# Optimization experiments

Hardware: AMD Instinct MI355X
Metric: run time of the kernel (lower is better)

Reference implementation:

```python
import jax, jax.numpy as jnp
import numpy as np

N = 20000      # nodes
E = 400000     # edges
D = 256        # input_dim == hidden_dim
L = 4          # num_layers
EIN = 32       # edgenet_input_dim // 2
EH = 128       # edge parser hidden
NC = 2         # num_classes
JK = L * D     # 1024
BN_EPS = 1e-5


def setup_inputs() -> dict:
    key = jax.random.key(0)
    ks = jax.random.split(key, 16)
    s = 0.05
    inp = {
        "features": jax.random.normal(ks[0], (N, D), jnp.float32),
        "edge_index": jax.random.randint(ks[1], (2, E), 0, N, dtype=jnp.int64),
        "edgenet_input": jax.random.normal(ks[2], (E, 2 * EIN), jnp.float32),
        # ChebConv weights: [layer, k, in, out] (all layers 256->256, K=3, no bias)
        "cheb_w": jax.random.normal(ks[3], (L, 3, D, D), jnp.float32) * s,
        # EdgeEncoder (PAE-style) parser: Linear(32,128)+ReLU+BN+Linear(128,128)
        "en_w1": jax.random.normal(ks[4], (EIN, EH), jnp.float32) * s,
        "en_b1": jnp.zeros((EH,), jnp.float32),
        "en_g1": jnp.ones((EH,), jnp.float32),
        "en_be1": jnp.zeros((EH,), jnp.float32),
        "en_w2": jax.random.normal(ks[5], (EH, EH), jnp.float32) * s,
        "en_b2": jnp.zeros((EH,), jnp.float32),
        # cls head: Linear(1024,256)+ReLU+BN(256)+Linear(256,2)
        "cls_w1": jax.random.normal(ks[6], (JK, 256), jnp.float32) * s,
        "cls_b1": jnp.zeros((256,), jnp.float32),
        "cls_g": jnp.ones((256,), jnp.float32),
        "cls_b": jnp.zeros((256,), jnp.float32),
        "cls_w2": jax.random.normal(ks[7], (256, NC), jnp.float32) * s,
        "cls_b2": jnp.zeros((NC,), jnp.float32),
    }
    return inp


def _bn_eval(x, g, b):
    # eval-mode BatchNorm1d with fresh running stats (mean=0, var=1)
    return x * (g / jnp.sqrt(1.0 + BN_EPS)) + b


def reference(features, edge_index, edgenet_input, cheb_w,
              en_w1, en_b1, en_g1, en_be1, en_w2, en_b2,
              cls_w1, cls_b1, cls_g, cls_b, cls_w2, cls_b2):
    row, col = edge_index[0], edge_index[1]

    # ---- EdgeEncoder (PAE): shared parser on both halves + cosine sim ----
    def parser(x):
        h = jnp.maximum(x @ en_w1 + en_b1, 0.0)
        h = _bn_eval(h, en_g1, en_be1)
        return h @ en_w2 + en_b2

    half = edgenet_input.shape[1] // 2
    h1 = parser(edgenet_input[:, :half])
    h2 = parser(edgenet_input[:, half:])
    n1 = jnp.maximum(jnp.linalg.norm(h1, axis=1), 1e-8)
    n2 = jnp.maximum(jnp.linalg.norm(h2, axis=1), 1e-8)
    cos = jnp.sum(h1 * h2, axis=1) / (n1 * n2)
    edge_weight = (cos + 1.0) * 0.5  # [E]

    # ---- ChebConv sym normalization (lambda_max=2): L_hat = -D^-1/2 A D^-1/2 ----
    deg = jax.ops.segment_sum(edge_weight, row, num_segments=N)
    dis = jnp.where(deg > 0, jax.lax.rsqrt(jnp.maximum(deg, 1e-30)), 0.0)
    norm = -dis[row] * edge_weight * dis[col]  # [E]

    def prop(x):  # out[col] += norm * x[row]
        return jax.ops.segment_sum(x[row] * norm[:, None], col, num_segments=N)

    # ---- stacked ChebConv (K=3, no bias) + ReLU + JK concat ----
    x = features
    jk = None
    for i in range(L):
        W = cheb_w[i]
        Tx0 = x
        Tx1 = prop(Tx0)
        Tx2 = 2.0 * prop(Tx1) - Tx0
        h = jnp.maximum(Tx0 @ W[0] + Tx1 @ W[1] + Tx2 @ W[2], 0.0)
        jk = h if i == 0 else jnp.concatenate([jk, h], axis=1)
        x = h

    # ---- cls head ----
    z = jnp.maximum(jk @ cls_w1 + cls_b1, 0.0)
    z = _bn_eval(z, cls_g, cls_b)
    logit = z @ cls_w2 + cls_b2
    return (logit, edge_weight)
```

## Files before the change

### kernel.cpp

```cpp
#include <hip/hip_runtime.h>
#include <hip/hip_bf16.h>

#define NN 20000
#define EE 400000
#define RSBN 0.9999950000374997f

typedef __attribute__((ext_vector_type(8))) short short8;
typedef __attribute__((ext_vector_type(8))) unsigned short ushort8;
typedef __attribute__((ext_vector_type(4))) short bf4;
typedef __attribute__((ext_vector_type(4))) float floatx4;

__device__ __forceinline__ short f2bf(float f) {
  union { float f; unsigned u; } v; v.f = f;
  unsigned r = v.u + 0x7fffu + ((v.u >> 16) & 1u);
  return (short)(r >> 16);
}
__device__ __forceinline__ unsigned f2bf2(float x, float y) {
  union { __hip_bfloat162 h; unsigned u; } v;
  v.h = __float22bfloat162_rn(make_float2(x, y));
  return v.u;
}
__device__ __forceinline__ float bf2f(unsigned short u) {
  union { unsigned u; float f; } v; v.u = ((unsigned)u) << 16;
  return v.f;
}
__device__ __forceinline__ void gl_lds16(const void* g, void* l) {
  __builtin_amdgcn_global_load_lds(
      (const __attribute__((address_space(1))) unsigned*)g,
      (__attribute__((address_space(3))) unsigned*)l, 16, 0, 0);
}

__device__ __forceinline__ floatx4 mfma16(bf4 a, bf4 b, floatx4 c) {
#if __has_builtin(__builtin_amdgcn_mfma_f32_16x16x16bf16_1k)
  return __builtin_amdgcn_mfma_f32_16x16x16bf16_1k(a, b, c, 0, 0, 0);
#else
  floatx4 d;
  asm volatile("v_mfma_f32_16x16x16_bf16 %0, %1, %2, %3"
               : "=&v"(d) : "v"(a), "v"(b), "v"(c));
  return d;
#endif
}

__device__ __forceinline__ float dpp_xor1(float x) {
  union { float f; int i; } a, b;
  a.f = x;
  b.i = __builtin_amdgcn_update_dpp(0, a.i, 0xB1, 0xF, 0xF, false);
  return b.f;
}

__global__ __launch_bounds__(256) void ewconv_kernel(
    const float* __restrict__ w1, const float* __restrict__ w2,
    const float* __restrict__ g1, const float* __restrict__ be1,
    const float* __restrict__ b1, const float* __restrict__ b2,
    unsigned short* __restrict__ ewf)
{
  int tid = threadIdx.x;
#pragma unroll
  for (int i = 0; i < 16; i++) {
    int idx = i * 256 + tid;
    int k = idx >> 7, n = idx & 127;
    int pos = ((n >> 4) * 64 + (k >> 3) * 16 + (n & 15)) * 8 + (k & 7);
    ewf[pos] = f2bf(w1[idx]);
  }
#pragma unroll
  for (int i = 0; i < 64; i++) {
    int idx = i * 256 + tid;
    int k = idx >> 7, n = idx & 127;
    int u = k >> 4, q = (k >> 2) & 3, j = k & 3;
    int t = n >> 4, l = n & 15;
    int pos = (((u * 8 + t) * 4 + q) * 16 + l) * 4 + j;
    ewf[4096 + pos] = f2bf(w2[idx] * g1[k] * RSBN);
  }
  float* fb = (float*)(ewf + 20480);
  if (tid < 128) {
    fb[tid] = b1[tid];
    float acc = b2[tid];
    for (int k = 0; k < 128; k++) acc += be1[k] * w2[k * 128 + tid] * g1[k] * RSBN;
    fb[128 + tid] = acc;
  }
}

__global__ __launch_bounds__(512, 4) void edge_kernel(
    const float* __restrict__ xin, const int* __restrict__ eidx,
    const unsigned short* __restrict__ ewf,
    float* __restrict__ ew_out,
    float* __restrict__ deg, int* __restrict__ cnt)
{
  __shared__ short wbuf[20992];

  int tid = threadIdx.x;
  int lane = tid & 63;
  int wv = tid >> 6;
  int l15 = lane & 15;
  int quad = lane >> 4;

#pragma unroll
  for (int i = 0; i < 5; i++)
    gl_lds16(ewf + (i * 512 + tid) * 8, &wbuf[(i * 512 + tid) * 8]);
  if (tid < 64)
    gl_lds16(ewf + (2560 + tid) * 8, &wbuf[(2560 + tid) * 8]);

  const short* w1f = wbuf;
  const short* w2f = wbuf + 4096;

  int rowA = blockIdx.x * 256 + wv * 16;
  int rowB = rowA + 128;

  short8 afA, afB;
  {
    const float* xpA = xin + (size_t)(rowA + l15) * 32 + quad * 8;
    const float* xpB = xin + (size_t)(rowB + l15) * 32 + quad * 8;
    float4 a0 = *(const float4*)xpA;
    float4 a1 = *(const float4*)(xpA + 4);
    float4 b0 = *(const float4*)xpB;
    float4 b1v = *(const float4*)(xpB + 4);
    union { short8 s; unsigned u[4]; } a, b;
    a.u[0] = f2bf2(a0.x, a0.y); a.u[1] = f2bf2(a0.z, a0.w);
    a.u[2] = f2bf2(a1.x, a1.y); a.u[3] = f2bf2(a1.z, a1.w);
    b.u[0] = f2bf2(b0.x, b0.y); b.u[1] = f2bf2(b0.z, b0.w);
    b.u[2] = f2bf2(b1v.x, b1v.y); b.u[3] = f2bf2(b1v.z, b1v.w);
    afA = a.s; afB = b.s;
  }

  __syncthreads();

  const float* fb = (const float*)(wbuf + 20480);

  floatx4 acc1A[8], acc1B[8];
#pragma unroll
  for (int t = 0; t < 8; t++) {
    floatx4 z = *(const floatx4*)&fb[t * 16 + quad * 4];
    short8 w1v = *(const short8*)&w1f[(t * 64 + lane) * 8];
    acc1A[t] = __builtin_amdgcn_mfma_f32_16x16x32_bf16(w1v, afA, z, 0, 0, 0);
    acc1B[t] = __builtin_amdgcn_mfma_f32_16x16x32_bf16(w1v, afB, z, 0, 0, 0);
  }

  bf4 pbA[8], pbB[8];
#pragma unroll
  for (int u = 0; u < 8; u++) {
    union { bf4 s; unsigned w[2]; } oa, ob;
    oa.w[0] = f2bf2(fmaxf(acc1A[u][0], 0.f), fmaxf(acc1A[u][1], 0.f));
    oa.w[1] = f2bf2(fmaxf(acc1A[u][2], 0.f), fmaxf(acc1A[u][3], 0.f));
    ob.w[0] = f2bf2(fmaxf(acc1B[u][0], 0.f), fmaxf(acc1B[u][1], 0.f));
    ob.w[1] = f2bf2(fmaxf(acc1B[u][2], 0.f), fmaxf(acc1B[u][3], 0.f));
    pbA[u] = oa.s; pbB[u] = ob.s;
  }

  floatx4 acc2A[8], acc2B[8];
#pragma unroll
  for (int t = 0; t < 8; t++) {
    floatx4 z2 = *(const floatx4*)&fb[128 + t * 16 + quad * 4];
    acc2A[t] = z2; acc2B[t] = z2;
  }
#pragma unroll
  for (int u = 0; u < 8; u++)
#pragma unroll
    for (int t = 0; t < 8; t++) {
      bf4 a4 = *(const bf4*)&w2f[((u * 8 + t) * 64 + lane) * 4];
      acc2A[t] = mfma16(a4, pbA[u], acc2A[t]);
      acc2B[t] = mfma16(a4, pbB[u], acc2B[t]);
    }

#pragma unroll
  for (int tile = 0; tile < 2; tile++) {
    floatx4* acc2 = tile ? acc2B : acc2A;
    int rowbase = tile ? rowB : rowA;
    float qq = 0.f, pp = 0.f;
#pragma unroll
    for (int t = 0; t < 8; t++)
#pragma unroll
      for (int r = 0; r < 4; r++) {
        float h = acc2[t][r];
        float hp = dpp_xor1(h);
        qq += h * h;
        pp += h * hp;
      }
    qq += __shfl_xor(qq, 16, 64);
    pp += __shfl_xor(pp, 16, 64);
    qq += __shfl_xor(qq, 32, 64);
    pp += __shfl_xor(pp, 32, 64);
    float rr = dpp_xor1(qq);

    if (quad == 0 && !(l15 & 1)) {
      int e = (rowbase + l15) >> 1;
      float n1 = fmaxf(sqrtf(qq), 1e-8f);
      float n2 = fmaxf(sqrtf(rr), 1e-8f);
      float w = (pp / (n1 * n2) + 1.f) * 0.5f;
      ew_out[e] = w;
      atomicAdd(deg + eidx[e], w);
      atomicAdd(cnt + eidx[EE + e], 1);
    }
  }
}

__global__ __launch_bounds__(256) void fconv_kernel(const float* __restrict__ src,
                                                    unsigned short* __restrict__ dst) {
  size_t i = ((size_t)blockIdx.x * 256 + threadIdx.x) * 8;
  float4 a = *(const float4*)(src + i);
  float4 b = *(const float4*)(src + i + 4);
  union { ushort8 s; unsigned u[4]; } o;
  o.u[0] = f2bf2(a.x, a.y); o.u[1] = f2bf2(a.z, a.w);
  o.u[2] = f2bf2(b.x, b.y); o.u[3] = f2bf2(b.z, b.w);
  *(ushort8*)(dst + i) = o.s;
}

__global__ __launch_bounds__(256) void wconv_kernel(
    const float* __restrict__ cheb_w, const float* __restrict__ cls_w1,
    unsigned short* __restrict__ wtc, unsigned short* __restrict__ clsT)
{
  __shared__ unsigned short tile[64][80];
  int z = blockIdx.z;
  const float* src; unsigned short* dst; int ldk;
  if (z < 12) {
    int l = z / 3, c = z % 3;
    src = cheb_w + (size_t)z * 65536;
    dst = wtc + (size_t)l * 196608 + c * 256;
    ldk = 768;
  } else {
    int c = z - 12;
    src = cls_w1 + (size_t)c * 65536;
    dst = clsT + c * 256;
    ldk = 1024;
  }
  int t = threadIdx.x;
  int k0 = blockIdx.x * 64, n0 = blockIdx.y * 64;
#pragma unroll
  for (int pass = 0; pass < 4; pass++) {
    int kk = pass * 16 + (t >> 4);
    int nl = (t & 15) * 4;
    float4 v = *(const float4*)(src + (size_t)(k0 + kk) * 256 + n0 + nl);
    tile[nl + 0][kk] = f2bf(v.x);
    tile[nl + 1][kk] = f2bf(v.y);
    tile[nl + 2][kk] = f2bf(v.z);
    tile[nl + 3][kk] = f2bf(v.w);
  }
  __syncthreads();
  int nl = t >> 2, kc = (t & 3) * 16;
  ushort8 v0 = *(const ushort8*)&tile[nl][kc];
  ushort8 v1 = *(const ushort8*)&tile[nl][kc + 8];
  unsigned short* dp = dst + (size_t)(n0 + nl) * ldk + k0 + kc;
  *(ushort8*)dp = v0;
  *(ushort8*)(dp + 8) = v1;
}

__global__ __launch_bounds__(1024) void scan_kernel(const int* __restrict__ cnt, int* __restrict__ ptr) {
  __shared__ int sums[1024];
  int tid = threadIdx.x;
  const int n = NN;
  const int chunk = (n + 1023) / 1024;
  int base = tid * chunk;
  int s = 0;
  for (int i = 0; i < chunk; i++) {
    int idx = base + i;
    if (idx < n) s += (cnt[idx] + 3) & ~3;
  }
  sums[tid] = s;
  __syncthreads();
  for (int off = 1; off < 1024; off <<= 1) {
    int v = (tid >= off) ? sums[tid - off] : 0;
    __syncthreads();
    sums[tid] += v;
    __syncthreads();
  }
  int run = (tid == 0) ? 0 : sums[tid - 1];
  for (int i = 0; i < chunk; i++) {
    int idx = base + i;
    if (idx < n) { ptr[idx] = run; run += (cnt[idx] + 3) & ~3; }
  }
  if (tid == 1023) ptr[n] = run;
}

__global__ __launch_bounds__(256) void hist_kernel(const int* __restrict__ cnt,
                                                   int* __restrict__ hist) {
  __shared__ int lh[64];
  int tid = threadIdx.x;
  if (tid < 64) lh[tid] = 0;
  __syncthreads();
  int i = blockIdx.x * 256 + tid;
  if (i < NN) {
    int b = (cnt[i] + 3) >> 2; if (b > 63) b = 63;
    atomicAdd(&lh[b], 1);
  }
  __syncthreads();
  if (tid < 64 && lh[tid]) atomicAdd(&hist[tid], lh[tid]);
}

__global__ void binscan_kernel(const int* __restrict__ hist,
                               int* __restrict__ binbase, int* __restrict__ binfill) {
  int tid = threadIdx.x;
  int v = hist[tid];
  int x = v;
#pragma unroll
  for (int off = 1; off < 64; off <<= 1) {
    int y = __shfl_up(x, off, 64);
    if (tid >= off) x += y;
  }
  binbase[tid] = x - v;
  binfill[tid] = 0;
}

__global__ __launch_bounds__(256) void perm_kernel(const int* __restrict__ cnt,
                                                   const int* __restrict__ binbase,
                                                   int* __restrict__ binfill,
                                                   int* __restrict__ perm) {
  __shared__ int lh[64], lbase[64];
  int tid = threadIdx.x;
  if (tid < 64) lh[tid] = 0;
  __syncthreads();
  int i = blockIdx.x * 256 + tid;
  int b = 0, local = 0;
  bool valid = (i < NN);
  if (valid) {
    b = (cnt[i] + 3) >> 2; if (b > 63) b = 63;
    local = atomicAdd(&lh[b], 1);
  }
  __syncthreads();
  if (tid < 64 && lh[tid]) lbase[tid] = atomicAdd(&binfill[tid], lh[tid]);
  __syncthreads();
  if (valid) perm[binbase[b] + lbase[b] + local] = i;
}

__global__ void fill_kernel(const int* __restrict__ eidx, const float* __restrict__ ew,
                            const float* __restrict__ deg, const int* __restrict__ ptr,
                            int* __restrict__ fill, int* __restrict__ cidx, float* __restrict__ cval) {
  int e = blockIdx.x * 256 + threadIdx.x;
  if (e < EE) {
    int r = eidx[e], c = eidx[EE + e];
    float dr = deg[r], dc = deg[c];
    float ir = dr > 0.f ? 1.f / sqrtf(fmaxf(dr, 1e-30f)) : 0.f;
    float ic = dc > 0.f ? 1.f / sqrtf(fmaxf(dc, 1e-30f)) : 0.f;
    float nv = -ir * ew[e] * ic;
    int pos = ptr[c] + atomicAdd(&fill[c], 1);
    cidx[pos] = r;
    cval[pos] = nv;
  }
}

__global__ __launch_bounds__(256) void prop_kernel(
    const unsigned short* __restrict__ x, int ldx,
    const int* __restrict__ cidx, const float* __restrict__ cval,
    const int* __restrict__ ptr, const int* __restrict__ perm,
    unsigned short* __restrict__ y, int ldy,
    float alpha, const unsigned short* __restrict__ sub, int ldsub)
{
  int sliceid = blockIdx.x & 7;
  int colslice = sliceid >> 1;
  int chunk = (blockIdx.x >> 3) * 2 + (sliceid & 1);
  int ci = chunk * 32 + (threadIdx.x >> 3);
  if (ci >= NN) return;
  int c = perm[ci];
  int d = colslice * 64 + (threadIdx.x & 7) * 8;
  int p0 = ptr[c], p1 = ptr[c + 1];
  float a[8] = {0.f, 0.f, 0.f, 0.f, 0.f, 0.f, 0.f, 0.f};

#define PLOAD(P, R, W, V0, V1, V2, V3)                                  \
  do {                                                                  \
    R = *(const int4*)(cidx + (P));                                     \
    W = *(const float4*)(cval + (P));                                   \
    V0 = *(const ushort8*)(x + (size_t)R.x * ldx + d);                  \
    V1 = *(const ushort8*)(x + (size_t)R.y * ldx + d);                  \
    V2 = *(const ushort8*)(x + (size_t)R.z * ldx + d);                  \
    V3 = *(const ushort8*)(x + (size_t)R.w * ldx + d);                  \
  } while (0)

#define PACC(W, V0, V1, V2, V3)                                         \
  do {                                                                  \
    _Pragma("unroll")                                                   \
    for (int j = 0; j < 8; j++)                                         \
      a[j] += W.x * bf2f(V0[j]) + W.y * bf2f(V1[j]) +                   \
              W.z * bf2f(V2[j]) + W.w * bf2f(V3[j]);                    \
  } while (0)

  if (p0 < p1) {
    int n4 = (p1 - p0) >> 2;
    int4 rA, rB; float4 wA, wB;
    ushort8 vA0, vA1, vA2, vA3, vB0, vB1, vB2, vB3;
    PLOAD(p0, rA, wA, vA0, vA1, vA2, vA3);
    if (n4 == 1) {
      PACC(wA, vA0, vA1, vA2, vA3);
    } else {
      PLOAD(p0 + 4, rB, wB, vB0, vB1, vB2, vB3);
      int p = p0 + 8;
      if (n4 & 1) {
        PACC(wA, vA0, vA1, vA2, vA3);
        PLOAD(p, rA, wA, vA0, vA1, vA2, vA3);
        p += 4;
      }
      for (; p < p1; p += 8) {
        PACC(wA, vA0, vA1, vA2, vA3);
        PLOAD(p, rA, wA, vA0, vA1, vA2, vA3);
        PACC(wB, vB0, vB1, vB2, vB3);
        PLOAD(p + 4, rB, wB, vB0, vB1, vB2, vB3);
      }
      PACC(wA, vA0, vA1, vA2, vA3);
      PACC(wB, vB0, vB1, vB2, vB3);
    }
  }
#undef PLOAD
#undef PACC

  union { ushort8 s; unsigned u[4]; } o;
  if (sub) {
    ushort8 sv = *(const ushort8*)(sub + (size_t)c * ldsub + d);
#pragma unroll
    for (int j = 0; j < 8; j += 2)
      o.u[j >> 1] = f2bf2(alpha * a[j] - bf2f(sv[j]), alpha * a[j + 1] - bf2f(sv[j + 1]));
  } else {
#pragma unroll
    for (int j = 0; j < 8; j += 2)
      o.u[j >> 1] = f2bf2(a[j], a[j + 1]);
  }
  *(ushort8*)(y + (size_t)c * ldy + d) = o.s;
}

__global__ __launch_bounds__(256, 4) void mgemm_kernel(
    const unsigned short* A0, const unsigned short* A1,
    const unsigned short* A2, const unsigned short* A3,
    int l0, int l1, int l2, int l3, int nchunks,
    const unsigned short* __restrict__ BT, int ldbt,
    unsigned short* __restrict__ Cb, float* __restrict__ Cf, int ldc, int M,
    const float* __restrict__ bias, const float* __restrict__ bng,
    const float* __restrict__ bnb)
{
  __shared__ short As[4 * 64 * 8];
  __shared__ short Bs[4 * 128 * 8];
  int tid = threadIdx.x;
  int lane = tid & 63;
  int wv = tid >> 6;
  int l15 = lane & 15, quad = lane >> 4;
  int wr = wv >> 1, wc = wv & 1;
  int m0 = blockIdx.x * 64, n0 = blockIdx.y * 128;

  const unsigned short* Ap[4] = {A0, A1, A2, A3};
  int Al[4] = {l0, l1, l2, l3};

  int arow = tid & 63, ac = tid >> 6;
  int brow = tid & 127, bc = tid >> 7;

  floatx4 acc[2][4];
#pragma unroll
  for (int mi = 0; mi < 2; mi++)
#pragma unroll
    for (int nj = 0; nj < 4; nj++) acc[mi][nj] = (floatx4){0.f, 0.f, 0.f, 0.f};

  for (int c = 0; c < nchunks; c++) {
    const unsigned short* Abase = Ap[c] + (size_t)(m0 + arow) * Al[c] + ac * 8;
    const unsigned short* Bbase = BT + (size_t)(n0 + brow) * ldbt + c * 256 + bc * 8;
#pragma unroll 1
    for (int kb = 0; kb < 256; kb += 32) {
      __syncthreads();
      gl_lds16(Abase + kb, &As[tid * 8]);
      gl_lds16(Bbase + kb, &Bs[tid * 8]);
      gl_lds16(Bbase + 16 + kb, &Bs[(tid + 256) * 8]);
      __syncthreads();
      short8 af[2], bfv[4];
#pragma unroll
      for (int mi = 0; mi < 2; mi++)
        af[mi] = *(const short8*)&As[(quad * 64 + wr * 32 + mi * 16 + l15) * 8];
#pragma unroll
      for (int nj = 0; nj < 4; nj++)
        bfv[nj] = *(const short8*)&Bs[(quad * 128 + wc * 64 + nj * 16 + l15) * 8];
#pragma unroll
      for (int nj = 0; nj < 4; nj++)
#pragma unroll
        for (int mi = 0; mi < 2; mi++)
          acc[mi][nj] = __builtin_amdgcn_mfma_f32_16x16x32_bf16(af[mi], bfv[nj], acc[mi][nj], 0, 0, 0);
    }
  }

  if (Cb) {
#pragma unroll
    for (int mi = 0; mi < 2; mi++)
#pragma unroll
      for (int r = 0; r < 4; r++) {
        int row = m0 + wr * 32 + mi * 16 + quad * 4 + r;
        if (row < M) {
#pragma unroll
          for (int nj = 0; nj < 4; nj++) {
            int col = n0 + wc * 64 + nj * 16 + l15;
            Cb[(size_t)row * ldc + col] = (unsigned short)f2bf(fmaxf(acc[mi][nj][r], 0.f));
          }
        }
      }
  } else {
    float bs[4], g[4], bb[4];
#pragma unroll
    for (int nj = 0; nj < 4; nj++) {
      int col = n0 + wc * 64 + nj * 16 + l15;
      bs[nj] = bias[col]; g[nj] = bng[col] * RSBN; bb[nj] = bnb[col];
    }
#pragma unroll
    for (int mi = 0; mi < 2; mi++)
#pragma unroll
      for (int r = 0; r < 4; r++) {
        int row = m0 + wr * 32 + mi * 16 + quad * 4 + r;
        if (row < M) {
#pragma unroll
          for (int nj = 0; nj < 4; nj++) {
            int col = n0 + wc * 64 + nj * 16 + l15;
            float v = fmaxf(acc[mi][nj][r] + bs[nj], 0.f) * g[nj] + bb[nj];
            Cf[(size_t)row * ldc + col] = v;
          }
        }
      }
  }
}

__global__ __launch_bounds__(256) void logit_kernel(
    const float* __restrict__ z, const float* __restrict__ w2,
    const float* __restrict__ b2, float* __restrict__ out)
{
  int node = blockIdx.x * 4 + (threadIdx.x >> 6);
  if (node >= NN) return;
  int lane = threadIdx.x & 63;
  int k = lane * 4;
  float4 zv = *(const float4*)(z + (size_t)node * 256 + k);
  float4 wa = *(const float4*)(w2 + k * 2);
  float4 wb = *(const float4*)(w2 + k * 2 + 4);
  float a0 = zv.x * wa.x + zv.y * wa.z + zv.z * wb.x + zv.w * wb.z;
  float a1 = zv.x * wa.y + zv.y * wa.w + zv.z * wb.y + zv.w * wb.w;
#pragma unroll
  for (int m = 32; m >= 1; m >>= 1) {
    a0 += __shfl_xor(a0, m, 64);
    a1 += __shfl_xor(a1, m, 64);
  }
  if (lane == 0) {
    out[(size_t)node * 2]     = a0 + b2[0];
    out[(size_t)node * 2 + 1] = a1 + b2[1];
  }
}

extern "C" void kernel_launch(void* const* d_in, const int* in_sizes, int n_in,
                              void* d_out, int out_size, void* d_ws, size_t ws_size,
                              hipStream_t stream) {
  const float* features = (const float*)d_in[0];
  const int*   eidx     = (const int*)d_in[1];
  const float* xin      = (const float*)d_in[2];
  const float* cheb_w   = (const float*)d_in[3];
  const float* en_w1    = (const float*)d_in[4];
  const float* en_b1    = (const float*)d_in[5];
  const float* en_g1    = (const float*)d_in[6];
  const float* en_be1   = (const float*)d_in[7];
  const float* en_w2    = (const float*)d_in[8];
  const float* en_b2    = (const float*)d_in[9];
  const float* cls_w1   = (const float*)d_in[10];
  const float* cls_b1   = (const float*)d_in[11];
  const float* cls_g    = (const float*)d_in[12];
  const float* cls_b    = (const float*)d_in[13];
  const float* cls_w2   = (const float*)d_in[14];
  const float* cls_b2   = (const float*)d_in[15];
  float* out = (float*)d_out;

  char* ws = (char*)d_ws;
  size_t off = 0;
  auto alloc = [&](size_t bytes) -> void* {
    void* p = ws + off;
    off += (bytes + 255) & ~(size_t)255;
    return p;
  };
  const int CSRN = EE + 4 * NN;
  float* deg  = (float*)alloc((size_t)NN * 4);
  int*   cnt  = (int*)  alloc((size_t)NN * 4);
  int*   fil  = (int*)  alloc((size_t)NN * 4);
  int*   hist = (int*)  alloc(64 * 4);
  float* cval = (float*)alloc((size_t)CSRN * 4);
  int*   cidx = (int*)  alloc((size_t)CSRN * 4);
  size_t zero_len = off;
  int*   ptr  = (int*)  alloc((size_t)(NN + 1) * 4);
  int*   perm = (int*)  alloc((size_t)NN * 4);
  int*   binbase = (int*)alloc(64 * 4);
  int*   binfill = (int*)alloc(64 * 4);
  unsigned short* featb = (unsigned short*)alloc((size_t)NN * 256 * 2);
  unsigned short* Tx1   = (unsigned short*)alloc((size_t)NN * 256 * 2);
  unsigned short* Tx2   = (unsigned short*)alloc((size_t)NN * 256 * 2);
  unsigned short* jk    = (unsigned short*)alloc((size_t)NN * 1024 * 2);
  float* zbuf = (float*)alloc((size_t)NN * 256 * 4);
  unsigned short* wtc   = (unsigned short*)alloc((size_t)4 * 196608 * 2);
  unsigned short* clsT  = (unsigned short*)alloc((size_t)256 * 1024 * 2);
  unsigned short* ewf   = (unsigned short*)alloc((size_t)20992 * 2);
  alloc(262144);

  float* ew = out + (size_t)NN * 2;

  hipMemsetAsync(deg, 0, zero_len, stream);

  ewconv_kernel<<<1, 256, 0, stream>>>(en_w1, en_w2, en_g1, en_be1, en_b1, en_b2, ewf);
  edge_kernel<<<3125, 512, 0, stream>>>(xin, eidx, ewf, ew, deg, cnt);
  fconv_kernel<<<2500, 256, 0, stream>>>(features, featb);
  wconv_kernel<<<dim3(4, 4, 16), 256, 0, stream>>>(cheb_w, cls_w1, wtc, clsT);
  scan_kernel<<<1, 1024, 0, stream>>>(cnt, ptr);
  hist_kernel<<<(NN + 255) / 256, 256, 0, stream>>>(cnt, hist);
  binscan_kernel<<<1, 64, 0, stream>>>(hist, binbase, binfill);
  perm_kernel<<<(NN + 255) / 256, 256, 0, stream>>>(cnt, binbase, binfill, perm);
  fill_kernel<<<(EE + 255) / 256, 256, 0, stream>>>(eidx, ew, deg, ptr, fil, cidx, cval);

  dim3 ggrid(313, 2);
  for (int i = 0; i < 4; i++) {
    const unsigned short* x = (i == 0) ? featb : (jk + (size_t)(i - 1) * 256);
    int ldx = (i == 0) ? 256 : 1024;
    prop_kernel<<<2504, 256, 0, stream>>>(x, ldx, cidx, cval, ptr, perm, Tx1, 256, 1.f, nullptr, 0);
    prop_kernel<<<2504, 256, 0, stream>>>(Tx1, 256, cidx, cval, ptr, perm, Tx2, 256, 2.f, x, ldx);
    mgemm_kernel<<<ggrid, 256, 0, stream>>>(x, Tx1, Tx2, nullptr, ldx, 256, 256, 0, 3,
                                            wtc + (size_t)i * 196608, 768,
                                            jk + (size_t)i * 256, nullptr, 1024, NN,
                                            nullptr, nullptr, nullptr);
  }

  mgemm_kernel<<<ggrid, 256, 0, stream>>>(jk, jk + 256, jk + 512, jk + 768,
                                          1024, 1024, 1024, 1024, 4, clsT, 1024,
                                          nullptr, zbuf, 256, NN,
                                          cls_b1, cls_g, cls_b);
  logit_kernel<<<NN / 4, 256, 0, stream>>>(zbuf, cls_w2, cls_b2, out);
}
```

Baseline: 648.2 us.

## Simplify prop gather loop, raise its occupancy, and XCD-swizzle GEMM blocks

```diff
diff --git a/kernel.cpp b/kernel.cpp
--- a/kernel.cpp
+++ b/kernel.cpp
@@ -46,6 +46,12 @@
   a.f = x;
   b.i = __builtin_amdgcn_update_dpp(0, a.i, 0xB1, 0xF, 0xF, false);
   return b.f;
+}
+
+__device__ __forceinline__ int xcd_swizzle(int bid, int nwg) {
+  int q = nwg >> 3, r = nwg & 7;
+  int x = bid & 7, o = bid >> 3;
+  return (x < r ? x * (q + 1) : r * (q + 1) + (x - r) * q) + o;
 }
 
 __global__ __launch_bounds__(256) void ewconv_kernel(
@@ -336,7 +342,7 @@
   }
 }
 
-__global__ __launch_bounds__(256) void prop_kernel(
+__global__ __launch_bounds__(256, 8) void prop_kernel(
     const unsigned short* __restrict__ x, int ldx,
     const int* __restrict__ cidx, const float* __restrict__ cval,
     const int* __restrict__ ptr, const int* __restrict__ perm,
@@ -353,51 +359,18 @@
   int p0 = ptr[c], p1 = ptr[c + 1];
   float a[8] = {0.f, 0.f, 0.f, 0.f, 0.f, 0.f, 0.f, 0.f};
 
-#define PLOAD(P, R, W, V0, V1, V2, V3)                                  \
-  do {                                                                  \
-    R = *(const int4*)(cidx + (P));                                     \
-    W = *(const float4*)(cval + (P));                                   \
-    V0 = *(const ushort8*)(x + (size_t)R.x * ldx + d);                  \
-    V1 = *(const ushort8*)(x + (size_t)R.y * ldx + d);                  \
-    V2 = *(const ushort8*)(x + (size_t)R.z * ldx + d);                  \
-    V3 = *(const ushort8*)(x + (size_t)R.w * ldx + d);                  \
-  } while (0)
-
-#define PACC(W, V0, V1, V2, V3)                                         \
-  do {                                                                  \
-    _Pragma("unroll")                                                   \
-    for (int j = 0; j < 8; j++)                                         \
-      a[j] += W.x * bf2f(V0[j]) + W.y * bf2f(V1[j]) +                   \
-              W.z * bf2f(V2[j]) + W.w * bf2f(V3[j]);                    \
-  } while (0)
-
-  if (p0 < p1) {
-    int n4 = (p1 - p0) >> 2;
-    int4 rA, rB; float4 wA, wB;
-    ushort8 vA0, vA1, vA2, vA3, vB0, vB1, vB2, vB3;
-    PLOAD(p0, rA, wA, vA0, vA1, vA2, vA3);
-    if (n4 == 1) {
-      PACC(wA, vA0, vA1, vA2, vA3);
-    } else {
-      PLOAD(p0 + 4, rB, wB, vB0, vB1, vB2, vB3);
-      int p = p0 + 8;
-      if (n4 & 1) {
-        PACC(wA, vA0, vA1, vA2, vA3);
-        PLOAD(p, rA, wA, vA0, vA1, vA2, vA3);
-        p += 4;
-      }
-      for (; p < p1; p += 8) {
-        PACC(wA, vA0, vA1, vA2, vA3);
-        PLOAD(p, rA, wA, vA0, vA1, vA2, vA3);
-        PACC(wB, vB0, vB1, vB2, vB3);
-        PLOAD(p + 4, rB, wB, vB0, vB1, vB2, vB3);
-      }
-      PACC(wA, vA0, vA1, vA2, vA3);
-      PACC(wB, vB0, vB1, vB2, vB3);
-    }
-  }
-#undef PLOAD
-#undef PACC
+  for (int p = p0; p < p1; p += 4) {
+    int4 r4 = *(const int4*)(cidx + p);
+    float4 w4 = *(const float4*)(cval + p);
+    ushort8 v0 = *(const ushort8*)(x + (size_t)r4.x * ldx + d);
+    ushort8 v1 = *(const ushort8*)(x + (size_t)r4.y * ldx + d);
+    ushort8 v2 = *(const ushort8*)(x + (size_t)r4.z * ldx + d);
+    ushort8 v3 = *(const ushort8*)(x + (size_t)r4.w * ldx + d);
+#pragma unroll
+    for (int j = 0; j < 8; j++)
+      a[j] += w4.x * bf2f(v0[j]) + w4.y * bf2f(v1[j]) +
+              w4.z * bf2f(v2[j]) + w4.w * bf2f(v3[j]);
+  }
 
   union { ushort8 s; unsigned u[4]; } o;
   if (sub) {
@@ -429,7 +402,8 @@
   int wv = tid >> 6;
   int l15 = lane & 15, quad = lane >> 4;
   int wr = wv >> 1, wc = wv & 1;
-  int m0 = blockIdx.x * 64, n0 = blockIdx.y * 128;
+  int bidx = xcd_swizzle(blockIdx.x, gridDim.x);
+  int m0 = bidx * 64, n0 = blockIdx.y * 128;
 
   const unsigned short* Ap[4] = {A0, A1, A2, A3};
   int Al[4] = {l0, l1, l2, l3};
```

Result: no change. 655.2 us (+1.1%).
